# Optimization experiments

Hardware: AMD Instinct MI355X
Metric: run time of the kernel (lower is better)

Reference implementation:

```python
import jax, jax.numpy as jnp
import numpy as np

N = 100000   # nodes
E = 1600000  # edges
EL = 200000  # decode pairs
D_IN, D_HID, D_OUT = 128, 128, 64


def setup_inputs() -> dict:
    key = jax.random.key(0)
    ks = jax.random.split(key, 9)
    x = jax.random.normal(ks[0], (N, D_IN), dtype=jnp.float32)
    edge_index = jax.random.randint(ks[1], (2, E), 0, N, dtype=jnp.int64)
    edge_label_index = jax.random.randint(ks[2], (2, EL), 0, N, dtype=jnp.int64)
    # GCNConv params: weight [in, out] (no bias inside linear), bias added after aggregation
    W1 = jax.random.normal(ks[3], (D_IN, D_HID), dtype=jnp.float32) / np.sqrt(D_IN)
    b1 = jnp.zeros((D_HID,), dtype=jnp.float32)
    W2 = jax.random.normal(ks[4], (D_HID, D_HID), dtype=jnp.float32) / np.sqrt(D_HID)
    b2 = jnp.zeros((D_HID,), dtype=jnp.float32)
    W3 = jax.random.normal(ks[5], (D_HID, D_OUT), dtype=jnp.float32) / np.sqrt(D_HID)
    b3 = jnp.zeros((D_OUT,), dtype=jnp.float32)
    return {"x": x, "edge_index": edge_index, "edge_label_index": edge_label_index,
            "W1": W1, "b1": b1, "W2": W2, "b2": b2, "W3": W3, "b3": b3}


def _gcn_norm(edge_index, num_nodes, dtype):
    # add self-loops, compute symmetric normalization deg^-1/2[src]*deg^-1/2[dst]
    loop = jnp.arange(num_nodes, dtype=edge_index.dtype)
    src = jnp.concatenate([edge_index[0], loop])
    dst = jnp.concatenate([edge_index[1], loop])
    deg = jax.ops.segment_sum(jnp.ones(src.shape, dtype=dtype), dst, num_segments=num_nodes)
    dinv = jax.lax.rsqrt(deg)  # deg >= 1 due to self-loops
    norm = dinv[src] * dinv[dst]
    return src, dst, norm


def _gcn_conv(h, W, b, src, dst, norm, num_nodes):
    h = h @ W                               # [N, out]
    msg = h[src] * norm[:, None]            # gather + scale  [E+N, out]
    out = jax.ops.segment_sum(msg, dst, num_segments=num_nodes)  # scatter-add
    return out + b


def reference(x, edge_index, edge_label_index, W1, b1, W2, b2, W3, b3):
    num_nodes = x.shape[0]
    src, dst, norm = _gcn_norm(edge_index, num_nodes, x.dtype)
    h = jax.nn.relu(_gcn_conv(x, W1, b1, src, dst, norm, num_nodes))
    h = jax.nn.relu(_gcn_conv(h, W2, b2, src, dst, norm, num_nodes))  # dropout is identity in eval
    z = _gcn_conv(h, W3, b3, src, dst, norm, num_nodes)
    # decode: dot product over candidate pairs
    return jnp.sum(z[edge_label_index[0]] * z[edge_label_index[1]], axis=-1)
```

## Files before the change

### kernel.cpp

```cpp
#include <hip/hip_runtime.h>
#include <hip/hip_bf16.h>

#define N_NODES 100000
#define N_EDGES 1600000
#define N_EL    200000

#define NB_SCAN ((N_NODES + 255) / 256)
#define CPAD 16
#define GT_GEMM ((N_NODES + 63) / 64)

typedef unsigned int uint32;
typedef unsigned short ushort16;
typedef __attribute__((ext_vector_type(8))) short short8;
typedef __attribute__((ext_vector_type(4))) float f32x4;

static __device__ __forceinline__ ushort16 f2bf(float f) {
    uint32 u = __float_as_uint(f);
    u += 0x7fffu + ((u >> 16) & 1u);
    return (ushort16)(u >> 16);
}
static __device__ __forceinline__ float bf_lo(uint32 p) { return __uint_as_float(p << 16); }
static __device__ __forceinline__ float bf_hi(uint32 p) { return __uint_as_float(p & 0xffff0000u); }
static __device__ __forceinline__ float bf2f(ushort16 h) { return __uint_as_float((uint32)h << 16); }

__global__ void k_scan1(const int* __restrict__ cpad, int* __restrict__ rowptr,
                        int* __restrict__ bsum, float* __restrict__ dinv) {
    __shared__ int s[256];
    int t = threadIdx.x;
    int i = blockIdx.x * 256 + t;
    int v = (i < N_NODES) ? cpad[(size_t)i * CPAD] : 0;
    if (i < N_NODES) dinv[i] = 1.0f / sqrtf((float)(v + 1));
    s[t] = v;
    __syncthreads();
    for (int off = 1; off < 256; off <<= 1) {
        int u = (t >= off) ? s[t - off] : 0;
        __syncthreads();
        s[t] += u;
        __syncthreads();
    }
    if (i < N_NODES) rowptr[i] = s[t] - v;
    if (t == 255) bsum[blockIdx.x] = s[255];
}

__global__ void k_scan2(const int* __restrict__ bsum, int* __restrict__ boff) {
    __shared__ int s[512];
    int t = threadIdx.x;
    int v = (t < NB_SCAN) ? bsum[t] : 0;
    s[t] = v;
    __syncthreads();
    for (int off = 1; off < 512; off <<= 1) {
        int u = (t >= off) ? s[t - off] : 0;
        __syncthreads();
        s[t] += u;
        __syncthreads();
    }
    if (t < NB_SCAN) boff[t] = s[t] - v;
    if (t == NB_SCAN - 1) boff[NB_SCAN] = s[t];
}

__global__ void k_scan3(int* __restrict__ rowptr, const int* __restrict__ boff) {
    int i = blockIdx.x * 256 + threadIdx.x;
    if (i < N_NODES) rowptr[i] += boff[blockIdx.x];
    if (i == 0) rowptr[N_NODES] = boff[NB_SCAN];
}

__global__ void k_fill2(const int* __restrict__ src, const int* __restrict__ dst,
                        const int* __restrict__ rowptr, const int* __restrict__ r,
                        int* __restrict__ col) {
    int e = blockIdx.x * blockDim.x + threadIdx.x;
    if (e >= N_EDGES) return;
    int pos = rowptr[dst[e]] + r[e];
    __builtin_nontemporal_store(src[e], &col[pos]);
}

static __device__ __forceinline__ short8 load_afrag(const float* arow, int off) {
    float4 a0 = *(const float4*)(arow + off);
    float4 a1 = *(const float4*)(arow + off + 4);
    short8 af;
    af[0] = (short)f2bf(a0.x); af[1] = (short)f2bf(a0.y);
    af[2] = (short)f2bf(a0.z); af[3] = (short)f2bf(a0.w);
    af[4] = (short)f2bf(a1.x); af[5] = (short)f2bf(a1.y);
    af[6] = (short)f2bf(a1.z); af[7] = (short)f2bf(a1.w);
    return af;
}
static __device__ __forceinline__ short8 load_afrag(const ushort16* arow, int off) {
    return *(const short8*)(arow + off);
}

template <int D, typename AT>
static __device__ __forceinline__ void gemm_body(int bid, const AT* __restrict__ A,
        const float* __restrict__ W, ushort16* __restrict__ C) {
    constexpr int NT = D / 16;
    __shared__ short sB[4 * NT * 64 * 8];

    int tid = threadIdx.x;

    for (int idx = tid; idx < 128 * D; idx += 256) {
        int k = idx / D;
        int n = idx % D;
        int kt = k >> 5, kr = k & 31;
        int q = kr >> 3, j = kr & 7;
        int nt = n >> 4, nn = n & 15;
        sB[(((kt * NT + nt) * 64) + q * 16 + nn) * 8 + j] = (short)f2bf(W[idx]);
    }
    __syncthreads();

    int w = tid >> 6;
    int l = tid & 63;
    int q = l >> 4;
    int nn15 = l & 15;
    int m0 = bid * 64 + w * 16;

    f32x4 acc[NT];
#pragma unroll
    for (int i = 0; i < NT; ++i) acc[i] = (f32x4){0.f, 0.f, 0.f, 0.f};

    int m = m0 + nn15;
    m = min(m, N_NODES - 1);
    const AT* arow = A + (size_t)m * 128;

#pragma unroll
    for (int kt = 0; kt < 4; ++kt) {
        short8 af = load_afrag(arow, kt * 32 + q * 8);
#pragma unroll
        for (int nt = 0; nt < NT; ++nt) {
            short8 bf = *(const short8*)&sB[((kt * NT + nt) * 64 + l) * 8];
            acc[nt] = __builtin_amdgcn_mfma_f32_16x16x32_bf16(af, bf, acc[nt], 0, 0, 0);
        }
    }

#pragma unroll
    for (int nt = 0; nt < NT; ++nt) {
#pragma unroll
        for (int r = 0; r < 4; ++r) {
            int node = m0 + q * 4 + r;
            if (node < N_NODES)
                C[(size_t)node * D + nt * 16 + nn15] = f2bf(acc[nt][r]);
        }
    }
}

template <int D, typename AT>
__global__ __launch_bounds__(256, 4) void k_gemm_mfma(const AT* __restrict__ A,
        const float* __restrict__ W, ushort16* __restrict__ C) {
    gemm_body<D, AT>(blockIdx.x, A, W, C);
}

__global__ __launch_bounds__(256, 4) void k_fat1(const float* __restrict__ A,
        const float* __restrict__ W, ushort16* __restrict__ C,
        const int* __restrict__ dst, int* __restrict__ cpad, int* __restrict__ r) {
    if (blockIdx.x < GT_GEMM) {
        gemm_body<128, float>(blockIdx.x, A, W, C);
    } else {
        int e = (blockIdx.x - GT_GEMM) * 256 + threadIdx.x;
        if (e < N_EDGES) r[e] = atomicAdd(&cpad[(size_t)dst[e] * CPAD], 1);
    }
}

template <bool RELU>
__global__ void k_gather128(const int* __restrict__ rowptr, const int* __restrict__ col,
                            const float* __restrict__ dinv, const uint32* __restrict__ t,
                            const float* __restrict__ b, uint32* __restrict__ outbuf) {
    __shared__ int   sc[4][64];
    __shared__ float sd[4][64];
    int tid = threadIdx.x;
    unsigned wid = (blockIdx.x * 256u + tid) >> 6;
    if (wid >= N_NODES) return;
    int w = tid >> 6;
    int lane = tid & 63;
    int beg = rowptr[wid], end = rowptr[wid + 1];
    float di = dinv[wid];
    uint32 p = t[(size_t)wid * 64 + lane];
    float ax = di * bf_lo(p), ay = di * bf_hi(p);
    for (int base = beg; base < end; base += 64) {
        int cnt = min(end - base, 64);
        int c = 0;
        if (lane < cnt) c = col[base + lane];
        sc[w][lane] = c;
        float cd = (lane < cnt) ? dinv[c] : 0.f;
        sd[w][lane] = cd;
        int nb = (cnt + 7) >> 3;
        for (int j8 = 0; j8 < nb; ++j8) {
            int j = j8 << 3;
            int s0 = sc[w][j+0], s1 = sc[w][j+1], s2 = sc[w][j+2], s3 = sc[w][j+3];
            int s4 = sc[w][j+4], s5 = sc[w][j+5], s6 = sc[w][j+6], s7 = sc[w][j+7];
            uint32 v0 = t[(size_t)s0 * 64 + lane];
            uint32 v1 = t[(size_t)s1 * 64 + lane];
            uint32 v2 = t[(size_t)s2 * 64 + lane];
            uint32 v3 = t[(size_t)s3 * 64 + lane];
            uint32 v4 = t[(size_t)s4 * 64 + lane];
            uint32 v5 = t[(size_t)s5 * 64 + lane];
            uint32 v6 = t[(size_t)s6 * 64 + lane];
            uint32 v7 = t[(size_t)s7 * 64 + lane];
            float d0 = sd[w][j+0], d1 = sd[w][j+1], d2 = sd[w][j+2], d3 = sd[w][j+3];
            float d4 = sd[w][j+4], d5 = sd[w][j+5], d6 = sd[w][j+6], d7 = sd[w][j+7];
            ax = fmaf(d0, bf_lo(v0), ax); ay = fmaf(d0, bf_hi(v0), ay);
            ax = fmaf(d1, bf_lo(v1), ax); ay = fmaf(d1, bf_hi(v1), ay);
            ax = fmaf(d2, bf_lo(v2), ax); ay = fmaf(d2, bf_hi(v2), ay);
            ax = fmaf(d3, bf_lo(v3), ax); ay = fmaf(d3, bf_hi(v3), ay);
            ax = fmaf(d4, bf_lo(v4), ax); ay = fmaf(d4, bf_hi(v4), ay);
            ax = fmaf(d5, bf_lo(v5), ax); ay = fmaf(d5, bf_hi(v5), ay);
            ax = fmaf(d6, bf_lo(v6), ax); ay = fmaf(d6, bf_hi(v6), ay);
            ax = fmaf(d7, bf_lo(v7), ax); ay = fmaf(d7, bf_hi(v7), ay);
        }
    }
    float2 bb = ((const float2*)b)[lane];
    float ox = di * ax + bb.x;
    float oy = di * ay + bb.y;
    if (RELU) { ox = fmaxf(ox, 0.f); oy = fmaxf(oy, 0.f); }
    __builtin_nontemporal_store((uint32)f2bf(ox) | ((uint32)f2bf(oy) << 16),
                                &outbuf[(size_t)wid * 64 + lane]);
}

template <bool RELU>
__global__ void k_gather64(const int* __restrict__ rowptr, const int* __restrict__ col,
                           const float* __restrict__ dinv, const ushort16* __restrict__ t,
                           const float* __restrict__ b, ushort16* __restrict__ outbuf) {
    __shared__ int   sc[4][64];
    __shared__ float sd[4][64];
    int tid = threadIdx.x;
    unsigned wid = (blockIdx.x * 256u + tid) >> 6;
    if (wid >= N_NODES) return;
    int w = tid >> 6;
    int lane = tid & 63;
    int beg = rowptr[wid], end = rowptr[wid + 1];
    float di = dinv[wid];
    float acc = di * bf2f(t[(size_t)wid * 64 + lane]);
    for (int base = beg; base < end; base += 64) {
        int cnt = min(end - base, 64);
        int c = 0;
        if (lane < cnt) c = col[base + lane];
        sc[w][lane] = c;
        float cd = (lane < cnt) ? dinv[c] : 0.f;
        sd[w][lane] = cd;
        int nb = (cnt + 7) >> 3;
        for (int j8 = 0; j8 < nb; ++j8) {
            int j = j8 << 3;
            int s0 = sc[w][j+0], s1 = sc[w][j+1], s2 = sc[w][j+2], s3 = sc[w][j+3];
            int s4 = sc[w][j+4], s5 = sc[w][j+5], s6 = sc[w][j+6], s7 = sc[w][j+7];
            float v0 = bf2f(t[(size_t)s0 * 64 + lane]);
            float v1 = bf2f(t[(size_t)s1 * 64 + lane]);
            float v2 = bf2f(t[(size_t)s2 * 64 + lane]);
            float v3 = bf2f(t[(size_t)s3 * 64 + lane]);
            float v4 = bf2f(t[(size_t)s4 * 64 + lane]);
            float v5 = bf2f(t[(size_t)s5 * 64 + lane]);
            float v6 = bf2f(t[(size_t)s6 * 64 + lane]);
            float v7 = bf2f(t[(size_t)s7 * 64 + lane]);
            float d0 = sd[w][j+0], d1 = sd[w][j+1], d2 = sd[w][j+2], d3 = sd[w][j+3];
            float d4 = sd[w][j+4], d5 = sd[w][j+5], d6 = sd[w][j+6], d7 = sd[w][j+7];
            acc = fmaf(d0, v0, acc); acc = fmaf(d1, v1, acc);
            acc = fmaf(d2, v2, acc); acc = fmaf(d3, v3, acc);
            acc = fmaf(d4, v4, acc); acc = fmaf(d5, v5, acc);
            acc = fmaf(d6, v6, acc); acc = fmaf(d7, v7, acc);
        }
    }
    float o = di * acc + b[lane];
    if (RELU) o = fmaxf(o, 0.f);
    __builtin_nontemporal_store(f2bf(o), &outbuf[(size_t)wid * 64 + lane]);
}

__global__ void k_decode(const int* __restrict__ eli, const ushort16* __restrict__ z,
                         float* __restrict__ out) {
    int e = blockIdx.x * blockDim.x + threadIdx.x;
    if (e >= N_EL) return;
    int a = eli[e];
    int b = eli[N_EL + e];
    const uint4* za = (const uint4*)(z + (size_t)a * 64);
    const uint4* zb = (const uint4*)(z + (size_t)b * 64);
    float acc = 0.0f;
#pragma unroll
    for (int i = 0; i < 8; ++i) {
        uint4 va = za[i], vb = zb[i];
        acc += bf_lo(va.x) * bf_lo(vb.x) + bf_hi(va.x) * bf_hi(vb.x);
        acc += bf_lo(va.y) * bf_lo(vb.y) + bf_hi(va.y) * bf_hi(vb.y);
        acc += bf_lo(va.z) * bf_lo(vb.z) + bf_hi(va.z) * bf_hi(vb.z);
        acc += bf_lo(va.w) * bf_lo(vb.w) + bf_hi(va.w) * bf_hi(vb.w);
    }
    out[e] = acc;
}

extern "C" void kernel_launch(void* const* d_in, const int* in_sizes, int n_in,
                              void* d_out, int out_size, void* d_ws, size_t ws_size,
                              hipStream_t stream) {
    const float* x   = (const float*)d_in[0];
    const int*   ei  = (const int*)d_in[1];
    const int*   eli = (const int*)d_in[2];
    const float* W1  = (const float*)d_in[3];
    const float* b1  = (const float*)d_in[4];
    const float* W2  = (const float*)d_in[5];
    const float* b2  = (const float*)d_in[6];
    const float* W3  = (const float*)d_in[7];
    const float* b3  = (const float*)d_in[8];
    float* out = (float*)d_out;

    const int* srcA = ei;
    const int* dstA = ei + N_EDGES;

    char* ws = (char*)d_ws;
    float*    dinv   = (float*)   (ws + 0);
    int*      rowptr = (int*)     (ws + (1024u << 10));
    int*      bsum   = (int*)     (ws + (1888u << 10));
    int*      boff   = (int*)     (ws + (1896u << 10));
    int*      col    = (int*)     (ws + (2048u << 10));
    int*      r      = (int*)     (ws + (9u << 20));
    ushort16* t      = (ushort16*)(ws + (16u << 20));
    ushort16* aggb   = (ushort16*)(ws + (48u << 20));
    int*      cpad   = (int*)     (ws + (80u << 20));

    const int B = 256;
    const int gE  = (N_EDGES + B - 1) / B;
    const int gG  = (N_NODES * 64 + B - 1) / B;
    const int gEL = (N_EL + B - 1) / B;

    hipMemsetAsync(cpad, 0, (size_t)N_NODES * CPAD * sizeof(int), stream);
    k_fat1<<<GT_GEMM + gE, B, 0, stream>>>(x, W1, t, dstA, cpad, r);
    k_scan1<<<NB_SCAN, 256, 0, stream>>>(cpad, rowptr, bsum, dinv);
    k_scan2<<<1, 512, 0, stream>>>(bsum, boff);
    k_scan3<<<NB_SCAN, 256, 0, stream>>>(rowptr, boff);
    k_fill2<<<gE, B, 0, stream>>>(srcA, dstA, rowptr, r, col);

    k_gather128<true><<<gG, B, 0, stream>>>(rowptr, col, dinv, (const uint32*)t, b1,
                                            (uint32*)aggb);
    k_gemm_mfma<128, ushort16><<<GT_GEMM, B, 0, stream>>>(aggb, W2, t);
    k_gather128<true><<<gG, B, 0, stream>>>(rowptr, col, dinv, (const uint32*)t, b2,
                                            (uint32*)aggb);
    k_gemm_mfma<64, ushort16><<<GT_GEMM, B, 0, stream>>>(aggb, W3, t);
    k_gather64<false><<<gG, B, 0, stream>>>(rowptr, col, dinv, t, b3, aggb);

    k_decode<<<gEL, B, 0, stream>>>(eli, aggb, out);
}
```

Baseline: 449.3 us.

## Fold source-side dinv scaling into GEMM epilogue and use unweighted gathers

The GEMM epilogues for layers 2 and 3 now pre-scale each output row by dinv[node], so the following gathers sum neighbour rows without reading dinv per neighbour or using per-edge FMAs. A zeroed sentinel row at index N_NODES replaces the zero weight for padded slots. Layer-3 output is written with row stride 128 so the sentinel row is shared, and the layer-1 GEMM blocks are interleaved with the rank-counting blocks in k_fat1. W staging into shared memory is also packed into short8 writes. The cost is some extra epilogue multiplies and a strided 64-wide layout in the last layer.

```diff
diff --git a/kernel.cpp b/kernel.cpp
--- a/kernel.cpp
+++ b/kernel.cpp
@@ -8,6 +8,7 @@
 #define NB_SCAN ((N_NODES + 255) / 256)
 #define CPAD 16
 #define GT_GEMM ((N_NODES + 63) / 64)
+#define GE_RANK ((N_EDGES + 255) / 256)
 
 typedef unsigned int uint32;
 typedef unsigned short ushort16;
@@ -87,21 +88,27 @@
     return *(const short8*)(arow + off);
 }
 
-template <int D, typename AT>
+template <int D, typename AT, bool SCALE, int OS>
 static __device__ __forceinline__ void gemm_body(int bid, const AT* __restrict__ A,
-        const float* __restrict__ W, ushort16* __restrict__ C) {
+        const float* __restrict__ W, const float* __restrict__ dinv,
+        ushort16* __restrict__ C) {
     constexpr int NT = D / 16;
+    constexpr int LNT = (NT == 8) ? 3 : 2;
     __shared__ short sB[4 * NT * 64 * 8];
 
     int tid = threadIdx.x;
 
-    for (int idx = tid; idx < 128 * D; idx += 256) {
-        int k = idx / D;
-        int n = idx % D;
-        int kt = k >> 5, kr = k & 31;
-        int q = kr >> 3, j = kr & 7;
-        int nt = n >> 4, nn = n & 15;
-        sB[(((kt * NT + nt) * 64) + q * 16 + nn) * 8 + j] = (short)f2bf(W[idx]);
+    constexpr int COMBOS = 4 * 4 * NT * 16;
+    for (int cc = tid; cc < COMBOS; cc += 256) {
+        int nn = cc & 15;
+        int nt = (cc >> 4) & (NT - 1);
+        int q  = (cc >> (4 + LNT)) & 3;
+        int kt = cc >> (6 + LNT);
+        short8 pk;
+#pragma unroll
+        for (int j = 0; j < 8; ++j)
+            pk[j] = (short)f2bf(W[(kt * 32 + q * 8 + j) * D + nt * 16 + nn]);
+        *(short8*)&sB[(((kt * NT + nt) * 64) + q * 16 + nn) * 8] = pk;
     }
     __syncthreads();
 
@@ -129,35 +136,45 @@
         }
     }
 
+    float4 dv;
+    if constexpr (SCALE) dv = *(const float4*)(dinv + m0 + 4 * q);
+    const float* dvp = (const float*)&dv;
 #pragma unroll
     for (int nt = 0; nt < NT; ++nt) {
 #pragma unroll
         for (int r = 0; r < 4; ++r) {
             int node = m0 + q * 4 + r;
-            if (node < N_NODES)
-                C[(size_t)node * D + nt * 16 + nn15] = f2bf(acc[nt][r]);
+            if (node < N_NODES) {
+                float val = acc[nt][r];
+                if constexpr (SCALE) val *= dvp[r];
+                C[(size_t)node * OS + nt * 16 + nn15] = f2bf(val);
+            }
         }
     }
 }
 
-template <int D, typename AT>
+template <int D, typename AT, bool SCALE, int OS>
 __global__ __launch_bounds__(256, 4) void k_gemm_mfma(const AT* __restrict__ A,
-        const float* __restrict__ W, ushort16* __restrict__ C) {
-    gemm_body<D, AT>(blockIdx.x, A, W, C);
+        const float* __restrict__ W, const float* __restrict__ dinv,
+        ushort16* __restrict__ C) {
+    gemm_body<D, AT, SCALE, OS>(blockIdx.x, A, W, dinv, C);
 }
 
 __global__ __launch_bounds__(256, 4) void k_fat1(const float* __restrict__ A,
         const float* __restrict__ W, ushort16* __restrict__ C,
         const int* __restrict__ dst, int* __restrict__ cpad, int* __restrict__ r) {
-    if (blockIdx.x < GT_GEMM) {
-        gemm_body<128, float>(blockIdx.x, A, W, C);
+    unsigned bid = blockIdx.x;
+    unsigned g = bid / 5u;
+    if (bid % 5u == 0u) {
+        gemm_body<128, float, false, 128>(g, A, W, nullptr, C);
     } else {
-        int e = (blockIdx.x - GT_GEMM) * 256 + threadIdx.x;
+        unsigned rid = g * 4u + (bid % 5u) - 1u;
+        unsigned e = rid * 256u + threadIdx.x;
         if (e < N_EDGES) r[e] = atomicAdd(&cpad[(size_t)dst[e] * CPAD], 1);
     }
 }
 
-template <bool RELU>
+template <bool RELU, bool WEIGHTED>
 __global__ void k_gather128(const int* __restrict__ rowptr, const int* __restrict__ col,
                             const float* __restrict__ dinv, const uint32* __restrict__ t,
                             const float* __restrict__ b, uint32* __restrict__ outbuf) {
@@ -171,14 +188,15 @@
     int beg = rowptr[wid], end = rowptr[wid + 1];
     float di = dinv[wid];
     uint32 p = t[(size_t)wid * 64 + lane];
-    float ax = di * bf_lo(p), ay = di * bf_hi(p);
+    float ax, ay;
+    if (WEIGHTED) { ax = di * bf_lo(p); ay = di * bf_hi(p); }
+    else          { ax = bf_lo(p);      ay = bf_hi(p);      }
     for (int base = beg; base < end; base += 64) {
         int cnt = min(end - base, 64);
-        int c = 0;
+        int c = WEIGHTED ? 0 : N_NODES;
         if (lane < cnt) c = col[base + lane];
         sc[w][lane] = c;
-        float cd = (lane < cnt) ? dinv[c] : 0.f;
-        sd[w][lane] = cd;
+        if (WEIGHTED) sd[w][lane] = (lane < cnt) ? dinv[c] : 0.f;
         int nb = (cnt + 7) >> 3;
         for (int j8 = 0; j8 < nb; ++j8) {
             int j = j8 << 3;
@@ -192,16 +210,23 @@
             uint32 v5 = t[(size_t)s5 * 64 + lane];
             uint32 v6 = t[(size_t)s6 * 64 + lane];
             uint32 v7 = t[(size_t)s7 * 64 + lane];
-            float d0 = sd[w][j+0], d1 = sd[w][j+1], d2 = sd[w][j+2], d3 = sd[w][j+3];
-            float d4 = sd[w][j+4], d5 = sd[w][j+5], d6 = sd[w][j+6], d7 = sd[w][j+7];
-            ax = fmaf(d0, bf_lo(v0), ax); ay = fmaf(d0, bf_hi(v0), ay);
-            ax = fmaf(d1, bf_lo(v1), ax); ay = fmaf(d1, bf_hi(v1), ay);
-            ax = fmaf(d2, bf_lo(v2), ax); ay = fmaf(d2, bf_hi(v2), ay);
-            ax = fmaf(d3, bf_lo(v3), ax); ay = fmaf(d3, bf_hi(v3), ay);
-            ax = fmaf(d4, bf_lo(v4), ax); ay = fmaf(d4, bf_hi(v4), ay);
-            ax = fmaf(d5, bf_lo(v5), ax); ay = fmaf(d5, bf_hi(v5), ay);
-            ax = fmaf(d6, bf_lo(v6), ax); ay = fmaf(d6, bf_hi(v6), ay);
-            ax = fmaf(d7, bf_lo(v7), ax); ay = fmaf(d7, bf_hi(v7), ay);
+            if (WEIGHTED) {
+                float d0 = sd[w][j+0], d1 = sd[w][j+1], d2 = sd[w][j+2], d3 = sd[w][j+3];
+                float d4 = sd[w][j+4], d5 = sd[w][j+5], d6 = sd[w][j+6], d7 = sd[w][j+7];
+                ax = fmaf(d0, bf_lo(v0), ax); ay = fmaf(d0, bf_hi(v0), ay);
+                ax = fmaf(d1, bf_lo(v1), ax); ay = fmaf(d1, bf_hi(v1), ay);
+                ax = fmaf(d2, bf_lo(v2), ax); ay = fmaf(d2, bf_hi(v2), ay);
+                ax = fmaf(d3, bf_lo(v3), ax); ay = fmaf(d3, bf_hi(v3), ay);
+                ax = fmaf(d4, bf_lo(v4), ax); ay = fmaf(d4, bf_hi(v4), ay);
+                ax = fmaf(d5, bf_lo(v5), ax); ay = fmaf(d5, bf_hi(v5), ay);
+                ax = fmaf(d6, bf_lo(v6), ax); ay = fmaf(d6, bf_hi(v6), ay);
+                ax = fmaf(d7, bf_lo(v7), ax); ay = fmaf(d7, bf_hi(v7), ay);
+            } else {
+                ax += (bf_lo(v0) + bf_lo(v1)) + (bf_lo(v2) + bf_lo(v3))
+                    + ((bf_lo(v4) + bf_lo(v5)) + (bf_lo(v6) + bf_lo(v7)));
+                ay += (bf_hi(v0) + bf_hi(v1)) + (bf_hi(v2) + bf_hi(v3))
+                    + ((bf_hi(v4) + bf_hi(v5)) + (bf_hi(v6) + bf_hi(v7)));
+            }
         }
     }
     float2 bb = ((const float2*)b)[lane];
@@ -216,8 +241,7 @@
 __global__ void k_gather64(const int* __restrict__ rowptr, const int* __restrict__ col,
                            const float* __restrict__ dinv, const ushort16* __restrict__ t,
                            const float* __restrict__ b, ushort16* __restrict__ outbuf) {
-    __shared__ int   sc[4][64];
-    __shared__ float sd[4][64];
+    __shared__ int sc[4][64];
     int tid = threadIdx.x;
     unsigned wid = (blockIdx.x * 256u + tid) >> 6;
     if (wid >= N_NODES) return;
@@ -225,33 +249,26 @@
     int lane = tid & 63;
     int beg = rowptr[wid], end = rowptr[wid + 1];
     float di = dinv[wid];
-    float acc = di * bf2f(t[(size_t)wid * 64 + lane]);
+    float acc = bf2f(t[(size_t)wid * 128 + lane]);
     for (int base = beg; base < end; base += 64) {
         int cnt = min(end - base, 64);
-        int c = 0;
+        int c = N_NODES;
         if (lane < cnt) c = col[base + lane];
         sc[w][lane] = c;
-        float cd = (lane < cnt) ? dinv[c] : 0.f;
-        sd[w][lane] = cd;
         int nb = (cnt + 7) >> 3;
         for (int j8 = 0; j8 < nb; ++j8) {
             int j = j8 << 3;
             int s0 = sc[w][j+0], s1 = sc[w][j+1], s2 = sc[w][j+2], s3 = sc[w][j+3];
             int s4 = sc[w][j+4], s5 = sc[w][j+5], s6 = sc[w][j+6], s7 = sc[w][j+7];
-            float v0 = bf2f(t[(size_t)s0 * 64 + lane]);
-            float v1 = bf2f(t[(size_t)s1 * 64 + lane]);
-            float v2 = bf2f(t[(size_t)s2 * 64 + lane]);
-            float v3 = bf2f(t[(size_t)s3 * 64 + lane]);
-            float v4 = bf2f(t[(size_t)s4 * 64 + lane]);
-            float v5 = bf2f(t[(size_t)s5 * 64 + lane]);
-            float v6 = bf2f(t[(size_t)s6 * 64 + lane]);
-            float v7 = bf2f(t[(size_t)s7 * 64 + lane]);
-            float d0 = sd[w][j+0], d1 = sd[w][j+1], d2 = sd[w][j+2], d3 = sd[w][j+3];
-            float d4 = sd[w][j+4], d5 = sd[w][j+5], d6 = sd[w][j+6], d7 = sd[w][j+7];
-            acc = fmaf(d0, v0, acc); acc = fmaf(d1, v1, acc);
-            acc = fmaf(d2, v2, acc); acc = fmaf(d3, v3, acc);
-            acc = fmaf(d4, v4, acc); acc = fmaf(d5, v5, acc);
-            acc = fmaf(d6, v6, acc); acc = fmaf(d7, v7, acc);
+            float v0 = bf2f(t[(size_t)s0 * 128 + lane]);
+            float v1 = bf2f(t[(size_t)s1 * 128 + lane]);
+            float v2 = bf2f(t[(size_t)s2 * 128 + lane]);
+            float v3 = bf2f(t[(size_t)s3 * 128 + lane]);
+            float v4 = bf2f(t[(size_t)s4 * 128 + lane]);
+            float v5 = bf2f(t[(size_t)s5 * 128 + lane]);
+            float v6 = bf2f(t[(size_t)s6 * 128 + lane]);
+            float v7 = bf2f(t[(size_t)s7 * 128 + lane]);
+            acc += (v0 + v1) + (v2 + v3) + ((v4 + v5) + (v6 + v7));
         }
     }
     float o = di * acc + b[lane];
@@ -308,23 +325,23 @@
     int*      cpad   = (int*)     (ws + (80u << 20));
 
     const int B = 256;
-    const int gE  = (N_EDGES + B - 1) / B;
     const int gG  = (N_NODES * 64 + B - 1) / B;
     const int gEL = (N_EL + B - 1) / B;
 
     hipMemsetAsync(cpad, 0, (size_t)N_NODES * CPAD * sizeof(int), stream);
-    k_fat1<<<GT_GEMM + gE, B, 0, stream>>>(x, W1, t, dstA, cpad, r);
+    hipMemsetAsync((char*)t + (size_t)N_NODES * 256, 0, 256, stream);
+    k_fat1<<<GT_GEMM + GE_RANK, B, 0, stream>>>(x, W1, t, dstA, cpad, r);
     k_scan1<<<NB_SCAN, 256, 0, stream>>>(cpad, rowptr, bsum, dinv);
     k_scan2<<<1, 512, 0, stream>>>(bsum, boff);
     k_scan3<<<NB_SCAN, 256, 0, stream>>>(rowptr, boff);
-    k_fill2<<<gE, B, 0, stream>>>(srcA, dstA, rowptr, r, col);
-
-    k_gather128<true><<<gG, B, 0, stream>>>(rowptr, col, dinv, (const uint32*)t, b1,
-                                            (uint32*)aggb);
-    k_gemm_mfma<128, ushort16><<<GT_GEMM, B, 0, stream>>>(aggb, W2, t);
-    k_gather128<true><<<gG, B, 0, stream>>>(rowptr, col, dinv, (const uint32*)t, b2,
-                                            (uint32*)aggb);
-    k_gemm_mfma<64, ushort16><<<GT_GEMM, B, 0, stream>>>(aggb, W3, t);
+    k_fill2<<<GE_RANK, B, 0, stream>>>(srcA, dstA, rowptr, r, col);
+
+    k_gather128<true, true><<<gG, B, 0, stream>>>(rowptr, col, dinv, (const uint32*)t,
+                                                  b1, (uint32*)aggb);
+    k_gemm_mfma<128, ushort16, true, 128><<<GT_GEMM, B, 0, stream>>>(aggb, W2, dinv, t);
+    k_gather128<true, false><<<gG, B, 0, stream>>>(rowptr, col, dinv, (const uint32*)t,
+                                                   b2, (uint32*)aggb);
+    k_gemm_mfma<64, ushort16, true, 128><<<GT_GEMM, B, 0, stream>>>(aggb, W3, dinv, t);
     k_gather64<false><<<gG, B, 0, stream>>>(rowptr, col, dinv, t, b3, aggb);
 
     k_decode<<<gEL, B, 0, stream>>>(eli, aggb, out);
```

After: 431.1 us. 1.04x faster.
